# Performance work log

Hardware: AMD Instinct MI355X
Metric: run time of the kernel (lower is better)

## Reference

```python
import jax, jax.numpy as jnp
import numpy as np

B, N, D, H, QV = 8, 1024, 64, 4, 32
C = 2 * D + 1          # combined_dim = 129
K = C // 8             # per-head qk dim = 16
M_PER = 512
M = B * M_PER
NEG = -9e15


def setup_inputs() -> dict:
    key = jax.random.key(0)
    ks = jax.random.split(key, 24)
    s = 0.05
    x = jax.random.normal(ks[0], (B, N, D + 1), jnp.float32)
    h = jax.random.normal(ks[1], (B, N, D), jnp.float32)
    query_vectors = jax.random.normal(ks[2], (M, QV), jnp.float32)
    adj = jax.random.randint(ks[3], (N, N), 0, 2, jnp.int32)
    # unique observed nodes per graph (mimics torch.where on an obs mask)
    perm = jax.vmap(lambda k: jax.random.permutation(k, N))(jax.random.split(ks[4], B))
    nodes_n = perm[:, :M_PER].reshape(-1).astype(jnp.int32)
    nodes_b = jnp.repeat(jnp.arange(B, dtype=jnp.int32), M_PER)
    # per-head attention projections, stacked over heads
    Wq = jax.random.normal(ks[5], (H, C, K), jnp.float32) * s
    bq = jax.random.normal(ks[6], (H, K), jnp.float32) * s
    Wk = jax.random.normal(ks[7], (H, C, K), jnp.float32) * s
    bk = jax.random.normal(ks[8], (H, K), jnp.float32) * s
    Wv = jax.random.normal(ks[9], (H, C, C), jnp.float32) * s
    bv = jax.random.normal(ks[10], (H, C), jnp.float32) * s
    # attentionMLP: Linear(H*C, C) -> ReLU -> Linear(C, C)
    W1 = jax.random.normal(ks[11], (H * C, C), jnp.float32) * s
    b1 = jax.random.normal(ks[12], (C,), jnp.float32) * s
    W2 = jax.random.normal(ks[13], (C, C), jnp.float32) * s
    b2 = jax.random.normal(ks[14], (C,), jnp.float32) * s
    # MLP_Param hypernetwork tensors: W[qvd, in=C, out=D], b[qvd, D]
    Wr = jax.random.normal(ks[15], (QV, C, D), jnp.float32) * s
    br = jax.random.normal(ks[16], (QV, D), jnp.float32) * s
    Wu = jax.random.normal(ks[17], (QV, C, D), jnp.float32) * s
    bu = jax.random.normal(ks[18], (QV, D), jnp.float32) * s
    Wc = jax.random.normal(ks[19], (QV, C, D), jnp.float32) * s
    bc = jax.random.normal(ks[20], (QV, D), jnp.float32) * s
    return dict(x=x, h=h, query_vectors=query_vectors, adj=adj,
                nodes_b=nodes_b, nodes_n=nodes_n,
                Wq=Wq, bq=bq, Wk=Wk, bk=bk, Wv=Wv, bv=bv,
                W1=W1, b1=b1, W2=W2, b2=b2,
                Wr=Wr, br=br, Wu=Wu, bu=bu, Wc=Wc, bc=bc)


def _mlp_param(sel, qv, W, b):
    # hypernetwork: per-node generated linear layer
    Wn = jnp.einsum('md,dio->mio', qv, W)   # [M, C, D]
    bn = qv @ b                              # [M, D]
    return jnp.einsum('mi,mio->mo', sel, Wn) + bn


def reference(x, h, query_vectors, adj, nodes_b, nodes_n,
              Wq, bq, Wk, bk, Wv, bv, W1, b1, W2, b2,
              Wr, br, Wu, bu, Wc, bc):
    combined = jnp.concatenate([x, h], axis=-1)                      # [B,N,C]
    q = jnp.einsum('bnc,hck->hbnk', combined, Wq) + bq[:, None, None, :]
    k = jnp.einsum('bnc,hck->hbnk', combined, Wk) + bk[:, None, None, :]
    v = jnp.einsum('bnc,hcd->hbnd', combined, Wv) + bv[:, None, None, :]
    scores = jnp.einsum('hbnk,hbmk->hbnm', q, k) / jnp.sqrt(jnp.float32(K))
    scores = jax.nn.leaky_relu(scores, 0.2)
    scores = jnp.where(adj == 0, NEG, scores)                        # [N,N] broadcast
    attn = jax.nn.softmax(scores, axis=-1)                           # [H,B,N,N]
    hp = jnp.einsum('hbnm,hbmd->hbnd', attn, v)                      # [H,B,N,C]
    # permute(1,2,0,3).reshape -> concat heads per node
    attn_cat = jnp.transpose(hp, (1, 2, 0, 3)).reshape(B, N, H * C)
    mlp_out = jax.nn.relu(attn_cat @ W1 + b1) @ W2 + b2              # [B,N,C]
    combined = mlp_out + combined                                    # skip connection
    sel = combined[nodes_b, nodes_n]                                 # [M,C]
    r = jax.nn.sigmoid(_mlp_param(sel, query_vectors, Wr, br))       # [M,D]
    u = jax.nn.sigmoid(_mlp_param(sel, query_vectors, Wu, bu))       # [M,D]
    h = h.at[nodes_b, nodes_n].set(r * h[nodes_b, nodes_n])
    combined_new = jnp.concatenate([x, h], axis=-1)
    cand = jnp.tanh(_mlp_param(combined_new[nodes_b, nodes_n], query_vectors, Wc, bc))
    new_h = (1.0 - u) * h[nodes_b, nodes_n] + u * cand               # [M,D]
    return new_h
```

## Files before the change

### kernel.cpp

```cpp
#include <hip/hip_runtime.h>

#define DEVINL __device__ __forceinline__

typedef unsigned short ushort_t;
typedef unsigned long long u64;
typedef __attribute__((ext_vector_type(8))) short short8;
typedef __attribute__((ext_vector_type(8))) unsigned short ushort8;
typedef __attribute__((ext_vector_type(4))) float f32x4;

constexpr int B_ = 8, N_ = 1024, D_ = 64, H_ = 4, QV_ = 32;
constexpr int C_ = 129, K_ = 16, M_ = 4096;
constexpr int CP = 132;
constexpr int NG = B_ * N_;
constexpr int CBS = 160;
constexpr int VTN = 144;
constexpr int KT = 4256;
constexpr int NKT = 133;
constexpr int HPS = 544;

constexpr size_t o_cb    = 0;
constexpr size_t o_qb    = o_cb  + (size_t)NG * CBS / 2;
constexpr size_t o_kb    = o_qb  + (size_t)H_ * NG * 16 / 2;
constexpr size_t o_adjb  = o_kb  + (size_t)H_ * NG * 16 / 2;
constexpr size_t o_wqk   = o_adjb + 32768;
constexpr size_t o_wvt   = o_wqk + (size_t)H_ * 32 * CBS / 2;
constexpr size_t o_vT    = o_wvt + (size_t)H_ * VTN * CBS / 2;
constexpr size_t o_hpb   = o_vT  + (size_t)H_ * VTN * NG / 2;
constexpr size_t o_cpost = o_hpb + (size_t)M_ * HPS / 2;
constexpr size_t o_W1T   = o_cpost + (size_t)M_ * CP;
constexpr size_t o_W2T   = o_W1T + (size_t)144 * HPS / 2;
constexpr size_t o_wtru  = o_W2T + (size_t)144 * 160 / 2;
constexpr size_t o_wtc   = o_wtru + (size_t)128 * KT / 2;
constexpr size_t o_A     = o_wtc + (size_t)64 * KT / 2;
constexpr size_t o_pru   = o_A + (size_t)M_ * KT / 2;
constexpr size_t o_pc2   = o_pru + (size_t)4 * M_ * 128;
constexpr size_t o_cin = o_vT;

DEVINL float4 ld4(const float* p) { return *reinterpret_cast<const float4*>(p); }
DEVINL void st4(float* p, float4 v) { *reinterpret_cast<float4*>(p) = v; }
DEVINL ushort_t f2bf(float f) {
    unsigned int u = __float_as_uint(f);
    u += 0x7FFFu + ((u >> 16) & 1u);
    return (ushort_t)(u >> 16);
}

__global__ void k_comb(const float* __restrict__ x, const float* __restrict__ h,
                       ushort_t* __restrict__ cb) {
    int idx = blockIdx.x * 256 + threadIdx.x;
    if (idx >= NG * CBS) return;
    int g = idx / CBS, kk = idx - g * CBS;
    float v;
    if (kk < 65) v = x[g * 65 + kk];
    else if (kk < 129) v = h[g * 64 + (kk - 65)];
    else if (kk == 129) v = 1.0f;
    else v = 0.f;
    cb[idx] = f2bf(v);
}

__global__ void k_adjb(const int* __restrict__ adj, u64* __restrict__ ab) {
    int word = blockIdx.x * 4 + (threadIdx.x >> 6);
    int lane = threadIdx.x & 63;
    int row = word >> 4, wj = word & 15;
    u64 m = __ballot(adj[(size_t)row * N_ + wj * 64 + lane] != 0);
    if (lane == 0) ab[word] = m;
}

__global__ void k_wqkv(const float* __restrict__ Wq, const float* __restrict__ bq,
                       const float* __restrict__ Wk, const float* __restrict__ bk,
                       const float* __restrict__ Wv, const float* __restrict__ bv,
                       ushort_t* __restrict__ wqk, ushort_t* __restrict__ wvt) {
    int idx = blockIdx.x * 256 + threadIdx.x;
    const int tot1 = H_ * 32 * CBS;
    const int tot2 = H_ * VTN * CBS;
    if (idx < tot1) {
        int hh = idx / (32 * CBS); int rem = idx - hh * 32 * CBS;
        int o = rem / CBS, kk = rem - o * CBS;
        float v = 0.f;
        if (o < 16) {
            if (kk < 129) v = Wq[(size_t)(hh * C_ + kk) * K_ + o];
            else if (kk == 129) v = bq[hh * K_ + o];
        } else {
            int o2 = o - 16;
            if (kk < 129) v = Wk[(size_t)(hh * C_ + kk) * K_ + o2];
            else if (kk == 129) v = bk[hh * K_ + o2];
        }
        wqk[idx] = f2bf(v);
    } else if (idx < tot1 + tot2) {
        int j = idx - tot1;
        int hh = j / (VTN * CBS); int rem = j - hh * VTN * CBS;
        int n = rem / CBS, kk = rem - n * CBS;
        float v = 0.f;
        if (n < C_) {
            if (kk < 129) v = Wv[(size_t)(hh * C_ + kk) * C_ + n];
            else if (kk == 129) v = bv[hh * C_ + n];
        }
        wvt[j] = f2bf(v);
    }
}

__global__ void k_wmlp(const float* __restrict__ W1, const float* __restrict__ W2,
                       ushort_t* __restrict__ W1T, ushort_t* __restrict__ W2T) {
    int idx = blockIdx.x * 256 + threadIdx.x;
    const int tot1 = 144 * HPS;
    const int tot2 = 144 * 160;
    if (idx < tot1) {
        int o = idx / HPS, k = idx - o * HPS;
        float v = (o < C_ && k < 516) ? W1[(size_t)k * C_ + o] : 0.f;
        W1T[idx] = f2bf(v);
    } else if (idx < tot1 + tot2) {
        int j = idx - tot1;
        int o = j / 160, k = j - o * 160;
        float v = (o < C_ && k < C_) ? W2[(size_t)k * C_ + o] : 0.f;
        W2T[j] = f2bf(v);
    }
}

__global__ void k_wt(const float* __restrict__ Wr, const float* __restrict__ br,
                     const float* __restrict__ Wu, const float* __restrict__ bu,
                     const float* __restrict__ Wc, const float* __restrict__ bc,
                     ushort_t* __restrict__ wtru, ushort_t* __restrict__ wtc) {
    int idx = blockIdx.x * 256 + threadIdx.x;
    const int tot = 192 * KT;
    if (idx >= tot) return;
    int row = idx / KT, k = idx - row * KT;
    float v;
    if (k >= 4224) {
        int d = k - 4224;
        if (row < 64) v = br[d * 64 + row];
        else if (row < 128) v = bu[d * 64 + row - 64];
        else v = bc[d * 64 + row - 128];
    } else {
        int d = k / 132, i = k - d * 132;
        if (i >= 129) v = 0.f;
        else if (row < 64) v = Wr[(size_t)(d * 129 + i) * 64 + row];
        else if (row < 128) v = Wu[(size_t)(d * 129 + i) * 64 + row - 64];
        else v = Wc[(size_t)(d * 129 + i) * 64 + row - 128];
    }
    if (row < 128) wtru[(size_t)row * KT + k] = f2bf(v);
    else wtc[(size_t)(row - 128) * KT + k] = f2bf(v);
}

__global__ __launch_bounds__(256) void k_qkv(
    const ushort_t* __restrict__ cb, const ushort_t* __restrict__ wqk,
    const ushort_t* __restrict__ wvt,
    ushort_t* __restrict__ qbo, ushort_t* __restrict__ kbo, ushort_t* __restrict__ vTg) {
    const int t = threadIdx.x;
    const int g0 = blockIdx.x * 16;
    const int hh = blockIdx.y;
    const int lane = t & 63, w = t >> 6;
    const int am = lane & 15, aq = lane >> 4;
    short8 cbf[5];
    const ushort_t* Cr = cb + (size_t)(g0 + am) * CBS + aq * 8;
#pragma unroll
    for (int kt = 0; kt < 5; ++kt)
        cbf[kt] = *reinterpret_cast<const short8*>(Cr + kt * 32);
#pragma unroll
    for (int s = 0; s < 3; ++s) {
        int u = w + 4 * s;
        if (u >= 11) break;
        f32x4 acc = f32x4{0.f, 0.f, 0.f, 0.f};
        if (u < 2) {
            const ushort_t* Bp = wqk + ((size_t)(hh * 32 + u * 16 + am)) * CBS + aq * 8;
#pragma unroll
            for (int kt = 0; kt < 5; ++kt)
                acc = __builtin_amdgcn_mfma_f32_16x16x32_bf16(
                    cbf[kt], *reinterpret_cast<const short8*>(Bp + kt * 32), acc, 0, 0, 0);
            ushort_t* dst = u ? kbo : qbo;
#pragma unroll
            for (int i = 0; i < 4; ++i)
                dst[(size_t)(hh * NG + g0 + aq * 4 + i) * 16 + am] = f2bf(acc[i]);
        } else {
            int vt = u - 2;
            const ushort_t* Ap = wvt + ((size_t)(hh * VTN + vt * 16 + am)) * CBS + aq * 8;
#pragma unroll
            for (int kt = 0; kt < 5; ++kt)
                acc = __builtin_amdgcn_mfma_f32_16x16x32_bf16(
                    *reinterpret_cast<const short8*>(Ap + kt * 32), cbf[kt], acc, 0, 0, 0);
#pragma unroll
            for (int i = 0; i < 4; ++i)
                vTg[(size_t)(hh * VTN + vt * 16 + aq * 4 + i) * NG + g0 + am] = f2bf(acc[i]);
        }
    }
}

__global__ __launch_bounds__(256) void k_attn(
    const ushort_t* __restrict__ qb, const ushort_t* __restrict__ kb,
    const ushort_t* __restrict__ vTg, const u64* __restrict__ adjb,
    const int* __restrict__ nodes_b, const int* __restrict__ nodes_n,
    ushort_t* __restrict__ hpb) {
    __shared__ u64 Msk[16][16];
    __shared__ alignas(16) ushort_t Pb[4][16 * 72];
    __shared__ float Ored[3][16 * 144];
    __shared__ float Lpart[4][16];
    __shared__ float Linv[16];
    __shared__ int Nrow[16];
    const int t = threadIdx.x;
    const int m0 = blockIdx.x * 16;
    const int hh = blockIdx.y;
    const int b = nodes_b[m0];
    if (t < 16) Nrow[t] = nodes_n[m0 + t];
    __syncthreads();
    { int r = t >> 4, wj = t & 15; Msk[r][wj] = adjb[Nrow[r] * 16 + wj]; }
    const int lane = t & 63, w = t >> 6;
    const int am = lane & 15, aq = lane >> 4;
    short8 qf = short8{0, 0, 0, 0, 0, 0, 0, 0};
    if (aq < 2)
        qf = *reinterpret_cast<const short8*>(&qb[(size_t)(hh * NG + b * N_ + Nrow[am]) * 16 + aq * 8]);
    __syncthreads();
    ushort_t* Pw = Pb[w];
    const ushort_t* kbase = kb + ((size_t)hh * NG + b * N_) * 16;
    f32x4 accv[9];
#pragma unroll
    for (int j = 0; j < 9; ++j) accv[j] = f32x4{0.f, 0.f, 0.f, 0.f};
    float lsum[4] = {0.f, 0.f, 0.f, 0.f};

    for (int ti = 0; ti < 4; ++ti) {
        const int c0 = (w + 4 * ti) * 64;
        u64 mrow[4];
#pragma unroll
        for (int i = 0; i < 4; ++i) mrow[i] = Msk[aq * 4 + i][c0 >> 6];
#pragma unroll
        for (int nt = 0; nt < 4; ++nt) {
            int col = c0 + nt * 16 + am;
            short8 bf = short8{0, 0, 0, 0, 0, 0, 0, 0};
            if (aq < 2)
                bf = *reinterpret_cast<const short8*>(&kbase[(size_t)col * 16 + aq * 8]);
            f32x4 sv = __builtin_amdgcn_mfma_f32_16x16x32_bf16(qf, bf, f32x4{0.f, 0.f, 0.f, 0.f}, 0, 0, 0);
#pragma unroll
            for (int i = 0; i < 4; ++i) {
                float s = sv[i] * 0.25f;
                s = (s >= 0.f) ? s : 0.2f * s;
                float p = ((mrow[i] >> (nt * 16 + am)) & 1ull) ? __expf(s) : 0.f;
                lsum[i] += p;
                Pw[(aq * 4 + i) * 72 + nt * 16 + am] = f2bf(p);
            }
        }
#pragma unroll
        for (int kh = 0; kh < 2; ++kh) {
            short8 af = *reinterpret_cast<const short8*>(&Pw[am * 72 + kh * 32 + aq * 8]);
#pragma unroll
            for (int nt = 0; nt < 9; ++nt) {
                short8 bfr = *reinterpret_cast<const short8*>(
                    &vTg[(size_t)(hh * VTN + nt * 16 + am) * NG + b * N_ + c0 + kh * 32 + aq * 8]);
                accv[nt] = __builtin_amdgcn_mfma_f32_16x16x32_bf16(af, bfr, accv[nt], 0, 0, 0);
            }
        }
    }
#pragma unroll
    for (int i = 0; i < 4; ++i) {
        float v = lsum[i];
        v += __shfl_xor(v, 1); v += __shfl_xor(v, 2);
        v += __shfl_xor(v, 4); v += __shfl_xor(v, 8);
        if (am == 0) Lpart[w][aq * 4 + i] = v;
    }
    if (w > 0) {
#pragma unroll
        for (int nt = 0; nt < 9; ++nt)
#pragma unroll
            for (int i = 0; i < 4; ++i)
                Ored[w - 1][(aq * 4 + i) * 144 + nt * 16 + am] = accv[nt][i];
    }
    __syncthreads();
    if (w == 0) {
        if (t < 16) {
            float s = Lpart[0][t] + Lpart[1][t] + Lpart[2][t] + Lpart[3][t];
            Linv[t] = (s > 0.f) ? 1.f / s : 0.f;
        }
#pragma unroll
        for (int nt = 0; nt < 9; ++nt) {
            int col = nt * 16 + am;
            if (col < C_) {
#pragma unroll
                for (int i = 0; i < 4; ++i) {
                    int row = aq * 4 + i;
                    float val = accv[nt][i] + Ored[0][row * 144 + col]
                              + Ored[1][row * 144 + col] + Ored[2][row * 144 + col];
                    hpb[(size_t)(m0 + row) * HPS + hh * C_ + col] = f2bf(val * Linv[row]);
                }
            }
        }
    }
    if (hh == 3) {
        for (int idx = t; idx < 16 * 28; idx += 256) {
            int rr = idx / 28, cc = 516 + (idx - rr * 28);
            hpb[(size_t)(m0 + rr) * HPS + cc] = 0;
        }
    }
}

__global__ __launch_bounds__(256) void k_mlp(
    const ushort_t* __restrict__ hpb,
    const ushort_t* __restrict__ W1T, const float* __restrict__ b1,
    const ushort_t* __restrict__ W2T, const float* __restrict__ b2,
    const float* __restrict__ x, const float* __restrict__ h,
    const int* __restrict__ nb, const int* __restrict__ nn,
    float* __restrict__ cpost) {
    __shared__ alignas(16) ushort_t Hs[16 * 168];
    const int t = threadIdx.x;
    const int m0 = blockIdx.x * 16;
    const int lane = t & 63, w = t >> 6;
    const int am = lane & 15, aq = lane >> 4;
    f32x4 acc[3];
#pragma unroll
    for (int j = 0; j < 3; ++j) acc[j] = f32x4{0.f, 0.f, 0.f, 0.f};
    const ushort_t* Ar = hpb + (size_t)(m0 + am) * HPS;
    for (int kt = 0; kt < 17; ++kt) {
        short8 af = *reinterpret_cast<const short8*>(Ar + kt * 32 + aq * 8);
#pragma unroll
        for (int j = 0; j < 3; ++j) {
            int nt = w + 4 * j;
            if (nt < 9) {
                short8 bf = *reinterpret_cast<const short8*>(W1T + (size_t)(nt * 16 + am) * HPS + kt * 32 + aq * 8);
                acc[j] = __builtin_amdgcn_mfma_f32_16x16x32_bf16(af, bf, acc[j], 0, 0, 0);
            }
        }
    }
#pragma unroll
    for (int j = 0; j < 3; ++j) {
        int nt = w + 4 * j;
        if (nt < 9) {
            int col = nt * 16 + am;
            float bb = (col < C_) ? b1[col] : 0.f;
#pragma unroll
            for (int i = 0; i < 4; ++i) {
                int row = aq * 4 + i;
                float v = (col < C_) ? fmaxf(acc[j][i] + bb, 0.f) : 0.f;
                Hs[row * 168 + col] = f2bf(v);
            }
        }
    }
    { int row = t >> 4, cc = 144 + (t & 15); Hs[row * 168 + cc] = 0; }
    __syncthreads();
    f32x4 acc2[3];
#pragma unroll
    for (int j = 0; j < 3; ++j) acc2[j] = f32x4{0.f, 0.f, 0.f, 0.f};
    for (int kt = 0; kt < 5; ++kt) {
        short8 af = *reinterpret_cast<const short8*>(&Hs[am * 168 + kt * 32 + aq * 8]);
#pragma unroll
        for (int j = 0; j < 3; ++j) {
            int nt = w + 4 * j;
            if (nt < 9) {
                short8 bf = *reinterpret_cast<const short8*>(W2T + (size_t)(nt * 16 + am) * 160 + kt * 32 + aq * 8);
                acc2[j] = __builtin_amdgcn_mfma_f32_16x16x32_bf16(af, bf, acc2[j], 0, 0, 0);
            }
        }
    }
#pragma unroll
    for (int j = 0; j < 3; ++j) {
        int nt = w + 4 * j;
        if (nt < 9) {
            int col = nt * 16 + am;
            if (col < C_) {
                float bb = b2[col];
#pragma unroll
                for (int i = 0; i < 4; ++i) {
                    int m = m0 + aq * 4 + i;
                    int b = nb[m], n = nn[m];
                    float sk = (col < 65) ? x[(b * N_ + n) * 65 + col]
                                          : h[(b * N_ + n) * D_ + (col - 65)];
                    cpost[(size_t)m * CP + col] = acc2[j][i] + bb + sk;
                }
            }
        }
    }
    if (t < 48) {
        int rr = t / 3, cc = 129 + (t - (t / 3) * 3);
        cpost[(size_t)(m0 + rr) * CP + cc] = 0.f;
    }
}

__global__ __launch_bounds__(256) void k_arow(const float* __restrict__ src,
                                              const float* __restrict__ qv,
                                              ushort_t* __restrict__ A) {
    __shared__ float sq[CP];
    __shared__ float qs[QV_];
    const int t = threadIdx.x;
    const int m = blockIdx.x;
    if (t < CP) sq[t] = src[(size_t)m * CP + t];
    if (t >= 224) qs[t - 224] = qv[m * QV_ + (t - 224)];
    __syncthreads();
    ushort_t* Ar = A + (size_t)m * KT;
    for (int k = t; k < 4224; k += 256) {
        int d = k / 132, i = k - d * 132;
        Ar[k] = f2bf(qs[d] * sq[i]);
    }
    if (t < QV_) Ar[4224 + t] = f2bf(qs[t]);
}

template<int NN>
__global__ __launch_bounds__(256) void k_gemm(const ushort_t* __restrict__ A,
                                              const ushort_t* __restrict__ WT,
                                              float* __restrict__ part) {
    const int t = threadIdx.x;
    const int m0 = blockIdx.x * 16;
    const int z = blockIdx.y;
    const int lane = t & 63, w = t >> 6;
    const int am = lane & 15, aq = lane >> 4;
    constexpr int NTpW = NN / 64;
    const int ktb = z * 34;
    const int kte = (ktb + 34 < NKT) ? ktb + 34 : NKT;
    f32x4 acc[NTpW];
#pragma unroll
    for (int j = 0; j < NTpW; ++j) acc[j] = f32x4{0.f, 0.f, 0.f, 0.f};
    const ushort_t* Ar = A + (size_t)(m0 + am) * KT;
    for (int kt = ktb; kt < kte; ++kt) {
        const int ko = kt * 32 + aq * 8;
        short8 af = *reinterpret_cast<const short8*>(Ar + ko);
#pragma unroll
        for (int j = 0; j < NTpW; ++j) {
            int nt = w + 4 * j;
            short8 bf = *reinterpret_cast<const short8*>(WT + (size_t)(nt * 16 + am) * KT + ko);
            acc[j] = __builtin_amdgcn_mfma_f32_16x16x32_bf16(af, bf, acc[j], 0, 0, 0);
        }
    }
#pragma unroll
    for (int j = 0; j < NTpW; ++j) {
        int n = (w + 4 * j) * 16 + am;
#pragma unroll
        for (int i = 0; i < 4; ++i) {
            int m = m0 + aq * 4 + i;
            part[((size_t)z * M_ + m) * NN + n] = acc[j][i];
        }
    }
}

__global__ void k_build_cin(const float* __restrict__ x, const float* __restrict__ h,
                            const int* __restrict__ nb, const int* __restrict__ nn,
                            const float* __restrict__ pru, float* __restrict__ cin) {
    int idx = blockIdx.x * 256 + threadIdx.x;
    if (idx >= M_ * CP) return;
    int m = idx / CP, i = idx - m * CP;
    int b = nb[m], n = nn[m];
    float val;
    if (i < 65) val = x[(b * N_ + n) * 65 + i];
    else if (i < C_) {
        int o = i - 65;
        const size_t S = (size_t)M_ * 128;
        size_t base = (size_t)m * 128 + o;
        float s = pru[base] + pru[S + base] + pru[2 * S + base] + pru[3 * S + base];
        float rv = 1.f / (1.f + __expf(-s));
        val = rv * h[(b * N_ + n) * D_ + o];
    } else val = 0.f;
    cin[idx] = val;
}

__global__ void k_final(const float* __restrict__ pru, const float* __restrict__ pc,
                        const float* __restrict__ cin, float* __restrict__ out) {
    int idx = blockIdx.x * 256 + threadIdx.x;
    if (idx >= M_ * D_) return;
    int m = idx >> 6, o = idx & 63;
    const size_t Su = (size_t)M_ * 128;
    size_t bu = (size_t)m * 128 + 64 + o;
    float su = pru[bu] + pru[Su + bu] + pru[2 * Su + bu] + pru[3 * Su + bu];
    float uv = 1.f / (1.f + __expf(-su));
    const size_t Sc = (size_t)M_ * 64;
    size_t bc = (size_t)m * 64 + o;
    float sc = pc[bc] + pc[Sc + bc] + pc[2 * Sc + bc] + pc[3 * Sc + bc];
    float cand = tanhf(sc);
    float hn = cin[(size_t)m * CP + 65 + o];
    out[idx] = (1.f - uv) * hn + uv * cand;
}

extern "C" void kernel_launch(void* const* d_in, const int* in_sizes, int n_in,
                              void* d_out, int out_size, void* d_ws, size_t ws_size,
                              hipStream_t stream) {
    const float* x   = (const float*)d_in[0];
    const float* h   = (const float*)d_in[1];
    const float* qv  = (const float*)d_in[2];
    const int*   adj = (const int*)d_in[3];
    const int*   nb  = (const int*)d_in[4];
    const int*   nn  = (const int*)d_in[5];
    const float* Wq  = (const float*)d_in[6];
    const float* bq  = (const float*)d_in[7];
    const float* Wk  = (const float*)d_in[8];
    const float* bk  = (const float*)d_in[9];
    const float* Wv  = (const float*)d_in[10];
    const float* bv  = (const float*)d_in[11];
    const float* W1  = (const float*)d_in[12];
    const float* b1  = (const float*)d_in[13];
    const float* W2  = (const float*)d_in[14];
    const float* b2  = (const float*)d_in[15];
    const float* Wr  = (const float*)d_in[16];
    const float* br  = (const float*)d_in[17];
    const float* Wu  = (const float*)d_in[18];
    const float* bu  = (const float*)d_in[19];
    const float* Wc  = (const float*)d_in[20];
    const float* bc  = (const float*)d_in[21];
    float* ws = (float*)d_ws;
    float* out = (float*)d_out;

    ushort_t* cb   = (ushort_t*)(ws + o_cb);
    ushort_t* qb   = (ushort_t*)(ws + o_qb);
    ushort_t* kb   = (ushort_t*)(ws + o_kb);
    u64*      ab   = (u64*)(ws + o_adjb);
    ushort_t* wqk  = (ushort_t*)(ws + o_wqk);
    ushort_t* wvt  = (ushort_t*)(ws + o_wvt);
    ushort_t* vTg  = (ushort_t*)(ws + o_vT);
    ushort_t* hpb  = (ushort_t*)(ws + o_hpb);
    float* cpost = ws + o_cpost;
    ushort_t* W1T  = (ushort_t*)(ws + o_W1T);
    ushort_t* W2T  = (ushort_t*)(ws + o_W2T);
    ushort_t* wtru = (ushort_t*)(ws + o_wtru);
    ushort_t* wtc  = (ushort_t*)(ws + o_wtc);
    ushort_t* Abuf = (ushort_t*)(ws + o_A);
    float* pru   = ws + o_pru;
    float* pc    = ws + o_pc2;
    float* cin   = ws + o_cin;

    k_comb<<<(NG * CBS + 255) / 256, 256, 0, stream>>>(x, h, cb);
    k_adjb<<<(N_ * 16) / 4, 256, 0, stream>>>(adj, ab);
    k_wqkv<<<(H_ * 32 * CBS + H_ * VTN * CBS + 255) / 256, 256, 0, stream>>>(
        Wq, bq, Wk, bk, Wv, bv, wqk, wvt);
    k_wmlp<<<(144 * HPS + 144 * 160 + 255) / 256, 256, 0, stream>>>(W1, W2, W1T, W2T);
    k_wt<<<(192 * KT + 255) / 256, 256, 0, stream>>>(Wr, br, Wu, bu, Wc, bc, wtru, wtc);
    k_qkv<<<dim3(NG / 16, H_), 256, 0, stream>>>(cb, wqk, wvt, qb, kb, vTg);
    k_attn<<<dim3(M_ / 16, H_), 256, 0, stream>>>(qb, kb, vTg, ab, nb, nn, hpb);
    k_mlp<<<M_ / 16, 256, 0, stream>>>(hpb, W1T, b1, W2T, b2, x, h, nb, nn, cpost);
    k_arow<<<M_, 256, 0, stream>>>(cpost, qv, Abuf);
    k_gemm<128><<<dim3(M_ / 16, 4), 256, 0, stream>>>(Abuf, wtru, pru);
    k_build_cin<<<(M_ * CP) / 256, 256, 0, stream>>>(x, h, nb, nn, pru, cin);
    k_arow<<<M_, 256, 0, stream>>>(cin, qv, Abuf);
    k_gemm<64><<<dim3(M_ / 16, 4), 256, 0, stream>>>(Abuf, wtc, pc);
    k_final<<<(M_ * D_) / 256, 256, 0, stream>>>(pru, pc, cin, out);
}
```

Measured before the change: 296.1 us.

## Split attention over key chunks with per-head waves and a separate merge kernel

```diff
diff --git a/kernel.cpp b/kernel.cpp
--- a/kernel.cpp
+++ b/kernel.cpp
@@ -34,7 +34,9 @@
 constexpr size_t o_A     = o_wtc + (size_t)64 * KT / 2;
 constexpr size_t o_pru   = o_A + (size_t)M_ * KT / 2;
 constexpr size_t o_pc2   = o_pru + (size_t)4 * M_ * 128;
-constexpr size_t o_cin = o_vT;
+constexpr size_t o_lpart = o_pc2 + (size_t)4 * M_ * 64;
+constexpr size_t o_cin   = o_vT;
+constexpr size_t o_opart = o_A;
 
 DEVINL float4 ld4(const float* p) { return *reinterpret_cast<const float4*>(p); }
 DEVINL void st4(float* p, float4 v) { *reinterpret_cast<float4*>(p) = v; }
@@ -187,38 +189,39 @@
     const ushort_t* __restrict__ qb, const ushort_t* __restrict__ kb,
     const ushort_t* __restrict__ vTg, const u64* __restrict__ adjb,
     const int* __restrict__ nodes_b, const int* __restrict__ nodes_n,
-    ushort_t* __restrict__ hpb) {
+    float* __restrict__ Opart, float* __restrict__ Lpart) {
     __shared__ u64 Msk[16][16];
     __shared__ alignas(16) ushort_t Pb[4][16 * 72];
-    __shared__ float Ored[3][16 * 144];
-    __shared__ float Lpart[4][16];
-    __shared__ float Linv[16];
     __shared__ int Nrow[16];
     const int t = threadIdx.x;
-    const int m0 = blockIdx.x * 16;
-    const int hh = blockIdx.y;
+    const int bi = blockIdx.x;
+    const int mx = (bi & 7) * 32 + (bi >> 3);
+    const int m0 = mx * 16;
+    const int z = blockIdx.y;
     const int b = nodes_b[m0];
     if (t < 16) Nrow[t] = nodes_n[m0 + t];
     __syncthreads();
     { int r = t >> 4, wj = t & 15; Msk[r][wj] = adjb[Nrow[r] * 16 + wj]; }
-    const int lane = t & 63, w = t >> 6;
+    const int lane = t & 63, hh = t >> 6;
     const int am = lane & 15, aq = lane >> 4;
     short8 qf = short8{0, 0, 0, 0, 0, 0, 0, 0};
     if (aq < 2)
         qf = *reinterpret_cast<const short8*>(&qb[(size_t)(hh * NG + b * N_ + Nrow[am]) * 16 + aq * 8]);
     __syncthreads();
-    ushort_t* Pw = Pb[w];
+    ushort_t* Pw = Pb[hh];
     const ushort_t* kbase = kb + ((size_t)hh * NG + b * N_) * 16;
     f32x4 accv[9];
 #pragma unroll
     for (int j = 0; j < 9; ++j) accv[j] = f32x4{0.f, 0.f, 0.f, 0.f};
     float lsum[4] = {0.f, 0.f, 0.f, 0.f};
 
+#pragma unroll
     for (int ti = 0; ti < 4; ++ti) {
-        const int c0 = (w + 4 * ti) * 64;
+        const int tile = z * 4 + ti;
+        const int c0 = tile * 64;
         u64 mrow[4];
 #pragma unroll
-        for (int i = 0; i < 4; ++i) mrow[i] = Msk[aq * 4 + i][c0 >> 6];
+        for (int i = 0; i < 4; ++i) mrow[i] = Msk[aq * 4 + i][tile];
 #pragma unroll
         for (int nt = 0; nt < 4; ++nt) {
             int col = c0 + nt * 16 + am;
@@ -251,40 +254,35 @@
         float v = lsum[i];
         v += __shfl_xor(v, 1); v += __shfl_xor(v, 2);
         v += __shfl_xor(v, 4); v += __shfl_xor(v, 8);
-        if (am == 0) Lpart[w][aq * 4 + i] = v;
-    }
-    if (w > 0) {
-#pragma unroll
-        for (int nt = 0; nt < 9; ++nt)
-#pragma unroll
-            for (int i = 0; i < 4; ++i)
-                Ored[w - 1][(aq * 4 + i) * 144 + nt * 16 + am] = accv[nt][i];
-    }
-    __syncthreads();
-    if (w == 0) {
-        if (t < 16) {
-            float s = Lpart[0][t] + Lpart[1][t] + Lpart[2][t] + Lpart[3][t];
-            Linv[t] = (s > 0.f) ? 1.f / s : 0.f;
-        }
-#pragma unroll
-        for (int nt = 0; nt < 9; ++nt) {
-            int col = nt * 16 + am;
-            if (col < C_) {
-#pragma unroll
-                for (int i = 0; i < 4; ++i) {
-                    int row = aq * 4 + i;
-                    float val = accv[nt][i] + Ored[0][row * 144 + col]
-                              + Ored[1][row * 144 + col] + Ored[2][row * 144 + col];
-                    hpb[(size_t)(m0 + row) * HPS + hh * C_ + col] = f2bf(val * Linv[row]);
-                }
-            }
-        }
-    }
-    if (hh == 3) {
-        for (int idx = t; idx < 16 * 28; idx += 256) {
-            int rr = idx / 28, cc = 516 + (idx - rr * 28);
-            hpb[(size_t)(m0 + rr) * HPS + cc] = 0;
-        }
+        if (am == 0) Lpart[((size_t)z * M_ + m0 + aq * 4 + i) * H_ + hh] = v;
+    }
+#pragma unroll
+    for (int nt = 0; nt < 9; ++nt)
+#pragma unroll
+        for (int i = 0; i < 4; ++i)
+            Opart[(((size_t)z * M_ + m0 + aq * 4 + i) * H_ + hh) * 144 + nt * 16 + am] = accv[nt][i];
+}
+
+__global__ void k_amerge(const float* __restrict__ Opart, const float* __restrict__ Lpart,
+                         ushort_t* __restrict__ hpb) {
+    int idx = blockIdx.x * 256 + threadIdx.x;
+    const int tot = M_ * H_ * 144;
+    if (idx < tot) {
+        int m = idx / (H_ * 144); int rem = idx - m * (H_ * 144);
+        int hh = rem / 144, col = rem - hh * 144;
+        if (col >= C_) return;
+        const size_t S = (size_t)M_ * H_ * 144;
+        size_t base = (size_t)idx;
+        float o = Opart[base] + Opart[S + base] + Opart[2 * S + base] + Opart[3 * S + base];
+        const size_t SL = (size_t)M_ * H_;
+        size_t lb = (size_t)m * H_ + hh;
+        float L = Lpart[lb] + Lpart[SL + lb] + Lpart[2 * SL + lb] + Lpart[3 * SL + lb];
+        float val = (L > 0.f) ? o / L : 0.f;
+        hpb[(size_t)m * HPS + hh * C_ + col] = f2bf(val);
+    } else if (idx < tot + M_ * 28) {
+        int j = idx - tot;
+        int m = j / 28, cc = 516 + (j - (j / 28) * 28);
+        hpb[(size_t)m * HPS + cc] = 0;
     }
 }
 
@@ -503,6 +501,8 @@
     ushort_t* wtru = (ushort_t*)(ws + o_wtru);
     ushort_t* wtc  = (ushort_t*)(ws + o_wtc);
     ushort_t* Abuf = (ushort_t*)(ws + o_A);
+    float* Opart = ws + o_opart;
+    float* Lpart = ws + o_lpart;
     float* pru   = ws + o_pru;
     float* pc    = ws + o_pc2;
     float* cin   = ws + o_cin;
@@ -514,7 +514,8 @@
     k_wmlp<<<(144 * HPS + 144 * 160 + 255) / 256, 256, 0, stream>>>(W1, W2, W1T, W2T);
     k_wt<<<(192 * KT + 255) / 256, 256, 0, stream>>>(Wr, br, Wu, bu, Wc, bc, wtru, wtc);
     k_qkv<<<dim3(NG / 16, H_), 256, 0, stream>>>(cb, wqk, wvt, qb, kb, vTg);
-    k_attn<<<dim3(M_ / 16, H_), 256, 0, stream>>>(qb, kb, vTg, ab, nb, nn, hpb);
+    k_attn<<<dim3(M_ / 16, 4), 256, 0, stream>>>(qb, kb, vTg, ab, nb, nn, Opart, Lpart);
+    k_amerge<<<(M_ * H_ * 144 + M_ * 28 + 255) / 256, 256, 0, stream>>>(Opart, Lpart, hpb);
     k_mlp<<<M_ / 16, 256, 0, stream>>>(hpb, W1T, b1, W2T, b2, x, h, nb, nn, cpost);
     k_arow<<<M_, 256, 0, stream>>>(cpost, qv, Abuf);
     k_gemm<128><<<dim3(M_ / 16, 4), 256, 0, stream>>>(Abuf, wtru, pru);
```

After: 306.6 us. 3.5% more time.

## Fuse prep kernels and build hypernetwork GEMM operand on the fly

Applied to the files above, without the earlier changes.

```diff
diff --git a/kernel.cpp b/kernel.cpp
--- a/kernel.cpp
+++ b/kernel.cpp
@@ -10,13 +10,12 @@
 
 constexpr int B_ = 8, N_ = 1024, D_ = 64, H_ = 4, QV_ = 32;
 constexpr int C_ = 129, K_ = 16, M_ = 4096;
-constexpr int CP = 132;
 constexpr int NG = B_ * N_;
 constexpr int CBS = 160;
 constexpr int VTN = 144;
-constexpr int KT = 4256;
-constexpr int NKT = 133;
+constexpr int KT2 = 5120;
 constexpr int HPS = 544;
+constexpr int SRS = 160;
 
 constexpr size_t o_cb    = 0;
 constexpr size_t o_qb    = o_cb  + (size_t)NG * CBS / 2;
@@ -27,14 +26,21 @@
 constexpr size_t o_vT    = o_wvt + (size_t)H_ * VTN * CBS / 2;
 constexpr size_t o_hpb   = o_vT  + (size_t)H_ * VTN * NG / 2;
 constexpr size_t o_cpost = o_hpb + (size_t)M_ * HPS / 2;
-constexpr size_t o_W1T   = o_cpost + (size_t)M_ * CP;
+constexpr size_t o_W1T   = o_cpost + (size_t)M_ * SRS;
 constexpr size_t o_W2T   = o_W1T + (size_t)144 * HPS / 2;
 constexpr size_t o_wtru  = o_W2T + (size_t)144 * 160 / 2;
-constexpr size_t o_wtc   = o_wtru + (size_t)128 * KT / 2;
-constexpr size_t o_A     = o_wtc + (size_t)64 * KT / 2;
-constexpr size_t o_pru   = o_A + (size_t)M_ * KT / 2;
+constexpr size_t o_wtc   = o_wtru + (size_t)128 * KT2 / 2;
+constexpr size_t o_pru   = o_wtc + (size_t)64 * KT2 / 2;
 constexpr size_t o_pc2   = o_pru + (size_t)4 * M_ * 128;
-constexpr size_t o_cin = o_vT;
+constexpr size_t o_cin   = o_vT;
+
+constexpr int SEG0 = NG * CBS;
+constexpr int SEG1 = SEG0 + H_ * 32 * CBS;
+constexpr int SEG2 = SEG1 + H_ * VTN * CBS;
+constexpr int SEG3 = SEG2 + 144 * HPS;
+constexpr int SEG4 = SEG3 + 144 * 160;
+constexpr int SEG5 = SEG4 + 192 * KT2;
+constexpr int SEG6 = SEG5 + 1024 * 16 * 64;
 
 DEVINL float4 ld4(const float* p) { return *reinterpret_cast<const float4*>(p); }
 DEVINL void st4(float* p, float4 v) { *reinterpret_cast<float4*>(p) = v; }
@@ -44,36 +50,31 @@
     return (ushort_t)(u >> 16);
 }
 
-__global__ void k_comb(const float* __restrict__ x, const float* __restrict__ h,
-                       ushort_t* __restrict__ cb) {
-    int idx = blockIdx.x * 256 + threadIdx.x;
-    if (idx >= NG * CBS) return;
-    int g = idx / CBS, kk = idx - g * CBS;
-    float v;
-    if (kk < 65) v = x[g * 65 + kk];
-    else if (kk < 129) v = h[g * 64 + (kk - 65)];
-    else if (kk == 129) v = 1.0f;
-    else v = 0.f;
-    cb[idx] = f2bf(v);
-}
-
-__global__ void k_adjb(const int* __restrict__ adj, u64* __restrict__ ab) {
-    int word = blockIdx.x * 4 + (threadIdx.x >> 6);
-    int lane = threadIdx.x & 63;
-    int row = word >> 4, wj = word & 15;
-    u64 m = __ballot(adj[(size_t)row * N_ + wj * 64 + lane] != 0);
-    if (lane == 0) ab[word] = m;
-}
-
-__global__ void k_wqkv(const float* __restrict__ Wq, const float* __restrict__ bq,
+__global__ void k_prep(const float* __restrict__ x, const float* __restrict__ h,
+                       const float* __restrict__ Wq, const float* __restrict__ bq,
                        const float* __restrict__ Wk, const float* __restrict__ bk,
                        const float* __restrict__ Wv, const float* __restrict__ bv,
-                       ushort_t* __restrict__ wqk, ushort_t* __restrict__ wvt) {
+                       const float* __restrict__ W1, const float* __restrict__ W2,
+                       const float* __restrict__ Wr, const float* __restrict__ br,
+                       const float* __restrict__ Wu, const float* __restrict__ bu,
+                       const float* __restrict__ Wc, const float* __restrict__ bc,
+                       const int* __restrict__ adj,
+                       ushort_t* __restrict__ cb, ushort_t* __restrict__ wqk,
+                       ushort_t* __restrict__ wvt, ushort_t* __restrict__ W1T,
+                       ushort_t* __restrict__ W2T, ushort_t* __restrict__ wtru,
+                       ushort_t* __restrict__ wtc, u64* __restrict__ ab) {
     int idx = blockIdx.x * 256 + threadIdx.x;
-    const int tot1 = H_ * 32 * CBS;
-    const int tot2 = H_ * VTN * CBS;
-    if (idx < tot1) {
-        int hh = idx / (32 * CBS); int rem = idx - hh * 32 * CBS;
+    if (idx < SEG0) {
+        int g = idx / CBS, kk = idx - g * CBS;
+        float v;
+        if (kk < 65) v = x[g * 65 + kk];
+        else if (kk < 129) v = h[g * 64 + (kk - 65)];
+        else if (kk == 129) v = 1.0f;
+        else v = 0.f;
+        cb[idx] = f2bf(v);
+    } else if (idx < SEG1) {
+        int j = idx - SEG0;
+        int hh = j / (32 * CBS); int rem = j - hh * 32 * CBS;
         int o = rem / CBS, kk = rem - o * CBS;
         float v = 0.f;
         if (o < 16) {
@@ -84,9 +85,9 @@
             if (kk < 129) v = Wk[(size_t)(hh * C_ + kk) * K_ + o2];
             else if (kk == 129) v = bk[hh * K_ + o2];
         }
-        wqk[idx] = f2bf(v);
-    } else if (idx < tot1 + tot2) {
-        int j = idx - tot1;
+        wqk[j] = f2bf(v);
+    } else if (idx < SEG2) {
+        int j = idx - SEG1;
         int hh = j / (VTN * CBS); int rem = j - hh * VTN * CBS;
         int n = rem / CBS, kk = rem - n * CBS;
         float v = 0.f;
@@ -95,49 +96,39 @@
             else if (kk == 129) v = bv[hh * C_ + n];
         }
         wvt[j] = f2bf(v);
-    }
-}
-
-__global__ void k_wmlp(const float* __restrict__ W1, const float* __restrict__ W2,
-                       ushort_t* __restrict__ W1T, ushort_t* __restrict__ W2T) {
-    int idx = blockIdx.x * 256 + threadIdx.x;
-    const int tot1 = 144 * HPS;
-    const int tot2 = 144 * 160;
-    if (idx < tot1) {
-        int o = idx / HPS, k = idx - o * HPS;
+    } else if (idx < SEG3) {
+        int j = idx - SEG2;
+        int o = j / HPS, k = j - o * HPS;
         float v = (o < C_ && k < 516) ? W1[(size_t)k * C_ + o] : 0.f;
-        W1T[idx] = f2bf(v);
-    } else if (idx < tot1 + tot2) {
-        int j = idx - tot1;
+        W1T[j] = f2bf(v);
+    } else if (idx < SEG4) {
+        int j = idx - SEG3;
         int o = j / 160, k = j - o * 160;
         float v = (o < C_ && k < C_) ? W2[(size_t)k * C_ + o] : 0.f;
         W2T[j] = f2bf(v);
-    }
-}
-
-__global__ void k_wt(const float* __restrict__ Wr, const float* __restrict__ br,
-                     const float* __restrict__ Wu, const float* __restrict__ bu,
-                     const float* __restrict__ Wc, const float* __restrict__ bc,
-                     ushort_t* __restrict__ wtru, ushort_t* __restrict__ wtc) {
-    int idx = blockIdx.x * 256 + threadIdx.x;
-    const int tot = 192 * KT;
-    if (idx >= tot) return;
-    int row = idx / KT, k = idx - row * KT;
-    float v;
-    if (k >= 4224) {
-        int d = k - 4224;
-        if (row < 64) v = br[d * 64 + row];
-        else if (row < 128) v = bu[d * 64 + row - 64];
-        else v = bc[d * 64 + row - 128];
-    } else {
-        int d = k / 132, i = k - d * 132;
-        if (i >= 129) v = 0.f;
-        else if (row < 64) v = Wr[(size_t)(d * 129 + i) * 64 + row];
-        else if (row < 128) v = Wu[(size_t)(d * 129 + i) * 64 + row - 64];
-        else v = Wc[(size_t)(d * 129 + i) * 64 + row - 128];
-    }
-    if (row < 128) wtru[(size_t)row * KT + k] = f2bf(v);
-    else wtc[(size_t)(row - 128) * KT + k] = f2bf(v);
+    } else if (idx < SEG5) {
+        int j = idx - SEG4;
+        int row = j / KT2, k = j - row * KT2;
+        int d = k / 160, i = k - d * 160;
+        float v = 0.f;
+        if (i < 129) {
+            if (row < 64) v = Wr[(size_t)(d * 129 + i) * 64 + row];
+            else if (row < 128) v = Wu[(size_t)(d * 129 + i) * 64 + row - 64];
+            else v = Wc[(size_t)(d * 129 + i) * 64 + row - 128];
+        } else if (i == 129) {
+            if (row < 64) v = br[d * 64 + row];
+            else if (row < 128) v = bu[d * 64 + row - 64];
+            else v = bc[d * 64 + row - 128];
+        }
+        if (row < 128) wtru[(size_t)row * KT2 + k] = f2bf(v);
+        else wtc[(size_t)(row - 128) * KT2 + k] = f2bf(v);
+    } else if (idx < SEG6) {
+        int j = idx - SEG5;
+        int word = j >> 6, lane = j & 63;
+        int row = word >> 4, wj = word & 15;
+        u64 m = __ballot(adj[(size_t)row * N_ + wj * 64 + lane] != 0);
+        if (lane == 0) ab[word] = m;
+    }
 }
 
 __global__ __launch_bounds__(256) void k_qkv(
@@ -215,10 +206,11 @@
     float lsum[4] = {0.f, 0.f, 0.f, 0.f};
 
     for (int ti = 0; ti < 4; ++ti) {
-        const int c0 = (w + 4 * ti) * 64;
+        const int tile = w + 4 * ti;
+        const int c0 = tile * 64;
         u64 mrow[4];
 #pragma unroll
-        for (int i = 0; i < 4; ++i) mrow[i] = Msk[aq * 4 + i][c0 >> 6];
+        for (int i = 0; i < 4; ++i) mrow[i] = Msk[aq * 4 + i][tile];
 #pragma unroll
         for (int nt = 0; nt < 4; ++nt) {
             int col = c0 + nt * 16 + am;
@@ -358,37 +350,20 @@
                     int b = nb[m], n = nn[m];
                     float sk = (col < 65) ? x[(b * N_ + n) * 65 + col]
                                           : h[(b * N_ + n) * D_ + (col - 65)];
-                    cpost[(size_t)m * CP + col] = acc2[j][i] + bb + sk;
+                    cpost[(size_t)m * SRS + col] = acc2[j][i] + bb + sk;
                 }
             }
         }
     }
-    if (t < 48) {
-        int rr = t / 3, cc = 129 + (t - (t / 3) * 3);
-        cpost[(size_t)(m0 + rr) * CP + cc] = 0.f;
-    }
-}
-
-__global__ __launch_bounds__(256) void k_arow(const float* __restrict__ src,
+    for (int idx = t; idx < 16 * 31; idx += 256) {
+        int rr = idx / 31, cc = 129 + (idx - (idx / 31) * 31);
+        cpost[(size_t)(m0 + rr) * SRS + cc] = (cc == 129) ? 1.f : 0.f;
+    }
+}
+
+template<int NN>
+__global__ __launch_bounds__(256) void k_gemm(const float* __restrict__ src,
                                               const float* __restrict__ qv,
-                                              ushort_t* __restrict__ A) {
-    __shared__ float sq[CP];
-    __shared__ float qs[QV_];
-    const int t = threadIdx.x;
-    const int m = blockIdx.x;
-    if (t < CP) sq[t] = src[(size_t)m * CP + t];
-    if (t >= 224) qs[t - 224] = qv[m * QV_ + (t - 224)];
-    __syncthreads();
-    ushort_t* Ar = A + (size_t)m * KT;
-    for (int k = t; k < 4224; k += 256) {
-        int d = k / 132, i = k - d * 132;
-        Ar[k] = f2bf(qs[d] * sq[i]);
-    }
-    if (t < QV_) Ar[4224 + t] = f2bf(qs[t]);
-}
-
-template<int NN>
-__global__ __launch_bounds__(256) void k_gemm(const ushort_t* __restrict__ A,
                                               const ushort_t* __restrict__ WT,
                                               float* __restrict__ part) {
     const int t = threadIdx.x;
@@ -397,19 +372,26 @@
     const int lane = t & 63, w = t >> 6;
     const int am = lane & 15, aq = lane >> 4;
     constexpr int NTpW = NN / 64;
-    const int ktb = z * 34;
-    const int kte = (ktb + 34 < NKT) ? ktb + 34 : NKT;
     f32x4 acc[NTpW];
 #pragma unroll
     for (int j = 0; j < NTpW; ++j) acc[j] = f32x4{0.f, 0.f, 0.f, 0.f};
-    const ushort_t* Ar = A + (size_t)(m0 + am) * KT;
-    for (int kt = ktb; kt < kte; ++kt) {
+    const float* Sr = src + (size_t)(m0 + am) * SRS;
+    const float* Qr = qv + (size_t)(m0 + am) * QV_;
+    for (int kt = z * 40; kt < z * 40 + 40; ++kt) {
+        const int d = kt / 5;
+        const int i0 = (kt - d * 5) * 32 + aq * 8;
+        const float qs = Qr[d];
+        float4 s0 = ld4(Sr + i0), s1 = ld4(Sr + i0 + 4);
+        short8 af;
+        af[0] = (short)f2bf(qs * s0.x); af[1] = (short)f2bf(qs * s0.y);
+        af[2] = (short)f2bf(qs * s0.z); af[3] = (short)f2bf(qs * s0.w);
+        af[4] = (short)f2bf(qs * s1.x); af[5] = (short)f2bf(qs * s1.y);
+        af[6] = (short)f2bf(qs * s1.z); af[7] = (short)f2bf(qs * s1.w);
         const int ko = kt * 32 + aq * 8;
-        short8 af = *reinterpret_cast<const short8*>(Ar + ko);
 #pragma unroll
         for (int j = 0; j < NTpW; ++j) {
             int nt = w + 4 * j;
-            short8 bf = *reinterpret_cast<const short8*>(WT + (size_t)(nt * 16 + am) * KT + ko);
+            short8 bf = *reinterpret_cast<const short8*>(WT + (size_t)(nt * 16 + am) * KT2 + ko);
             acc[j] = __builtin_amdgcn_mfma_f32_16x16x32_bf16(af, bf, acc[j], 0, 0, 0);
         }
     }
@@ -428,19 +410,20 @@
                             const int* __restrict__ nb, const int* __restrict__ nn,
                             const float* __restrict__ pru, float* __restrict__ cin) {
     int idx = blockIdx.x * 256 + threadIdx.x;
-    if (idx >= M_ * CP) return;
-    int m = idx / CP, i = idx - m * CP;
+    if (idx >= M_ * SRS) return;
+    int m = idx / SRS, i = idx - m * SRS;
     int b = nb[m], n = nn[m];
     float val;
     if (i < 65) val = x[(b * N_ + n) * 65 + i];
-    else if (i < C_) {
+    else if (i < 129) {
         int o = i - 65;
         const size_t S = (size_t)M_ * 128;
         size_t base = (size_t)m * 128 + o;
         float s = pru[base] + pru[S + base] + pru[2 * S + base] + pru[3 * S + base];
         float rv = 1.f / (1.f + __expf(-s));
         val = rv * h[(b * N_ + n) * D_ + o];
-    } else val = 0.f;
+    } else if (i == 129) val = 1.0f;
+    else val = 0.f;
     cin[idx] = val;
 }
 
@@ -457,7 +440,7 @@
     size_t bc = (size_t)m * 64 + o;
     float sc = pc[bc] + pc[Sc + bc] + pc[2 * Sc + bc] + pc[3 * Sc + bc];
     float cand = tanhf(sc);
-    float hn = cin[(size_t)m * CP + 65 + o];
+    float hn = cin[(size_t)m * SRS + 65 + o];
     out[idx] = (1.f - uv) * hn + uv * cand;
 }
 
@@ -502,24 +485,18 @@
     ushort_t* W2T  = (ushort_t*)(ws + o_W2T);
     ushort_t* wtru = (ushort_t*)(ws + o_wtru);
     ushort_t* wtc  = (ushort_t*)(ws + o_wtc);
-    ushort_t* Abuf = (ushort_t*)(ws + o_A);
     float* pru   = ws + o_pru;
     float* pc    = ws + o_pc2;
     float* cin   = ws + o_cin;
 
-    k_comb<<<(NG * CBS + 255) / 256, 256, 0, stream>>>(x, h, cb);
-    k_adjb<<<(N_ * 16) / 4, 256, 0, stream>>>(adj, ab);
-    k_wqkv<<<(H_ * 32 * CBS + H_ * VTN * CBS + 255) / 256, 256, 0, stream>>>(
-        Wq, bq, Wk, bk, Wv, bv, wqk, wvt);
-    k_wmlp<<<(144 * HPS + 144 * 160 + 255) / 256, 256, 0, stream>>>(W1, W2, W1T, W2T);
-    k_wt<<<(192 * KT + 255) / 256, 256, 0, stream>>>(Wr, br, Wu, bu, Wc, bc, wtru, wtc);
+    k_prep<<<(SEG6 + 255) / 256, 256, 0, stream>>>(
+        x, h, Wq, bq, Wk, bk, Wv, bv, W1, W2, Wr, br, Wu, bu, Wc, bc, adj,
+        cb, wqk, wvt, W1T, W2T, wtru, wtc, ab);
     k_qkv<<<dim3(NG / 16, H_), 256, 0, stream>>>(cb, wqk, wvt, qb, kb, vTg);
     k_attn<<<dim3(M_ / 16, H_), 256, 0, stream>>>(qb, kb, vTg, ab, nb, nn, hpb);
     k_mlp<<<M_ / 16, 256, 0, stream>>>(hpb, W1T, b1, W2T, b2, x, h, nb, nn, cpost);
-    k_arow<<<M_, 256, 0, stream>>>(cpost, qv, Abuf);
-    k_gemm<128><<<dim3(M_ / 16, 4), 256, 0, stream>>>(Abuf, wtru, pru);
-    k_build_cin<<<(M_ * CP) / 256, 256, 0, stream>>>(x, h, nb, nn, pru, cin);
-    k_arow<<<M_, 256, 0, stream>>>(cin, qv, Abuf);
-    k_gemm<64><<<dim3(M_ / 16, 4), 256, 0, stream>>>(Abuf, wtc, pc);
+    k_gemm<128><<<dim3(M_ / 16, 4), 256, 0, stream>>>(cpost, qv, wtru, pru);
+    k_build_cin<<<(M_ * SRS + 255) / 256, 256, 0, stream>>>(x, h, nb, nn, pru, cin);
+    k_gemm<64><<<dim3(M_ / 16, 4), 256, 0, stream>>>(cin, qv, wtc, pc);
     k_final<<<(M_ * D_) / 256, 256, 0, stream>>>(pru, pc, cin, out);
 }
```

Result: slower. 377.5 us (+27.5%).
